# Optimization experiments

Measured on AMD Instinct MI355X. Metric: run time of the kernel, lower is better.

Reference implementation:

```python
import jax, jax.numpy as jnp
import numpy as np

N_NODES = 50000
N_EDGES = 1000000
D_IN = 128
HID = 64
N_GRAPHS = 256
NEG_SLOPE = 0.2


def _gatv2_layer(x, src, dst, Wl, Wr, att, b, n_nodes):
    # lin_l applied to source nodes, lin_r to target nodes (PyG GATv2Conv, heads=1)
    xl = x @ Wl.T  # [N, C]
    xr = x @ Wr.T  # [N, C]
    e = jax.nn.leaky_relu(xl[src] + xr[dst], NEG_SLOPE)  # [E, C]
    logits = e @ att  # [E]
    # segment softmax over destination node
    m = jax.ops.segment_max(logits, dst, num_segments=n_nodes)
    ex = jnp.exp(logits - m[dst])
    den = jax.ops.segment_sum(ex, dst, num_segments=n_nodes)
    alpha = ex / den[dst]  # [E]
    out = jax.ops.segment_sum(alpha[:, None] * xl[src], dst, num_segments=n_nodes)
    return out + b


def setup_inputs() -> dict:
    key = jax.random.key(0)
    ks = jax.random.split(key, 32)
    x = jax.random.normal(ks[0], (N_NODES, D_IN), dtype=jnp.float32)
    edge_index = jax.random.randint(ks[1], (2, N_EDGES), 0, N_NODES, dtype=jnp.int64)
    batch = jnp.sort(jax.random.randint(ks[2], (N_NODES,), 0, N_GRAPHS, dtype=jnp.int64))
    inp = {"x": x, "edge_index": edge_index, "batch": batch}
    dims = [D_IN, HID, HID]  # input dim per layer
    kidx = 3
    for i, din in enumerate(dims):
        inp[f"Wl{i}"] = jax.random.normal(ks[kidx], (HID, din), dtype=jnp.float32) * 0.1; kidx += 1
        inp[f"Wr{i}"] = jax.random.normal(ks[kidx], (HID, din), dtype=jnp.float32) * 0.1; kidx += 1
        inp[f"att{i}"] = jax.random.normal(ks[kidx], (HID,), dtype=jnp.float32) * 0.1; kidx += 1
        inp[f"b{i}"] = jnp.zeros((HID,), dtype=jnp.float32)
        inp[f"Rw{i}"] = jax.random.normal(ks[kidx], (HID, din), dtype=jnp.float32) * 0.1; kidx += 1
        inp[f"Rb{i}"] = jnp.zeros((HID,), dtype=jnp.float32)
    inp["Wf"] = jax.random.normal(ks[kidx], (1, HID), dtype=jnp.float32) * 0.1
    inp["bf"] = jnp.zeros((1,), dtype=jnp.float32)
    return inp


def reference(x, edge_index, batch, Wl0, Wr0, att0, b0, Rw0, Rb0,
              Wl1, Wr1, att1, b1, Rw1, Rb1,
              Wl2, Wr2, att2, b2, Rw2, Rb2, Wf, bf):
    n = x.shape[0]
    # add_self_loops=True (PyG default)
    loops = jnp.arange(n, dtype=edge_index.dtype)
    src = jnp.concatenate([edge_index[0], loops])
    dst = jnp.concatenate([edge_index[1], loops])
    layers = [(Wl0, Wr0, att0, b0, Rw0, Rb0),
              (Wl1, Wr1, att1, b1, Rw1, Rb1),
              (Wl2, Wr2, att2, b2, Rw2, Rb2)]
    for i, (Wl, Wr, att, b, Rw, Rb) in enumerate(layers):
        h = _gatv2_layer(x, src, dst, Wl, Wr, att, b, n) + (x @ Rw.T + Rb)  # res=True
        # norm=None -> Identity; dropout inactive at inference
        x = jax.nn.relu(h) if i < len(layers) - 1 else h
    # global_mean_pool
    sums = jax.ops.segment_sum(x, batch, num_segments=N_GRAPHS)
    cnt = jax.ops.segment_sum(jnp.ones((n,), x.dtype), batch, num_segments=N_GRAPHS)
    pooled = sums / jnp.maximum(cnt, 1.0)[:, None]
    return pooled @ Wf.T + bf
```

## Files before the change

### kernel.cpp

```cpp
#include <hip/hip_runtime.h>


#define NN 50000
#define NE 1000000
#define HID 64
#define DIN0 128
#define NG 256
#define NEG 0.2f

#define SCHUNK 1024
#define SNB ((NN + SCHUNK - 1) / SCHUNK)

typedef float f32x4 __attribute__((ext_vector_type(4)));
typedef short s8v __attribute__((ext_vector_type(8)));
typedef short s4v __attribute__((ext_vector_type(4)));
typedef __bf16 bf16x8 __attribute__((ext_vector_type(8)));
typedef _Float16 h2v __attribute__((ext_vector_type(2)));
typedef unsigned u32x2 __attribute__((ext_vector_type(2)));
typedef unsigned short u16;

__device__ __forceinline__ unsigned short f2bf(float f) {
    unsigned u = __float_as_uint(f);
    u = u + 0x7fffu + ((u >> 16) & 1u);
    return (unsigned short)(u >> 16);
}
__device__ __forceinline__ float bf2f(unsigned short v) {
    return __uint_as_float(((unsigned)v) << 16);
}
__device__ __forceinline__ short split_hi(float x) {
    return (short)f2bf(x);
}
__device__ __forceinline__ short split_lo(float x, short hi) {
    return (short)f2bf(x - bf2f((unsigned short)hi));
}
__device__ __forceinline__ h2v u2h(unsigned u) { return __builtin_bit_cast(h2v, u); }
__device__ __forceinline__ unsigned h2u(h2v h) { return __builtin_bit_cast(unsigned, h); }
__device__ __forceinline__ h2v pklo(unsigned a, unsigned b) {
    return u2h(__builtin_amdgcn_perm(b, a, 0x05040100u));
}
__device__ __forceinline__ h2v pkhi(unsigned a, unsigned b) {
    return u2h(__builtin_amdgcn_perm(b, a, 0x07060302u));
}
template <int CTRL>
__device__ __forceinline__ float dpp_mv(float v) {
    return __int_as_float(
        __builtin_amdgcn_update_dpp(0, __float_as_int(v), CTRL, 0xF, 0xF, true));
}
template <int OFF>
__device__ __forceinline__ float swz(float v) {
    return __int_as_float(__builtin_amdgcn_ds_swizzle(__float_as_int(v), OFF));
}
__device__ __forceinline__ float red32_add(float v) {
    unsigned u = __float_as_uint(v);
    u32x2 r = __builtin_amdgcn_permlane32_swap(u, u, false, false);
    return __uint_as_float(r[0]) + __uint_as_float(r[1]);
}
__device__ __forceinline__ float red32_max(float v) {
    unsigned u = __float_as_uint(v);
    u32x2 r = __builtin_amdgcn_permlane32_swap(u, u, false, false);
    return fmaxf(__uint_as_float(r[0]), __uint_as_float(r[1]));
}
__device__ __forceinline__ float octet_sum(float v) {
    v += dpp_mv<0xB1>(v);
    v += dpp_mv<0x4E>(v);
    v += swz<0x101F>(v);
    return v;
}
__device__ __forceinline__ float esum(float v) {
    v += dpp_mv<0x128>(v);
    v += swz<0x401F>(v);
    return red32_add(v);
}
__device__ __forceinline__ float emax(float v) {
    v = fmaxf(v, dpp_mv<0x128>(v));
    v = fmaxf(v, swz<0x401F>(v));
    return red32_max(v);
}

__global__ __launch_bounds__(256) void k_prep(
        const float* __restrict__ Wl0, const float* __restrict__ Wr0, const float* __restrict__ Rw0,
        const float* __restrict__ Wl1, const float* __restrict__ Wr1, const float* __restrict__ Rw1,
        const float* __restrict__ Wl2, const float* __restrict__ Wr2, const float* __restrict__ Rw2,
        const float* __restrict__ att0, const float* __restrict__ att1, const float* __restrict__ att2,
        short* __restrict__ Ws0, short* __restrict__ Ws1, short* __restrict__ Ws2,
        _Float16* __restrict__ attp,
        const int* __restrict__ batch,
        int* __restrict__ startg, int* __restrict__ endg,
        int* __restrict__ cnt8) {
    int i = blockIdx.x * 256 + threadIdx.x;
    if (i < 3 * HID) {
        int L = i >> 6, c = i & 63;
        const float* at = (L == 0) ? att0 : (L == 1) ? att1 : att2;
        float a = at[c];
        attp[L * 2 * HID + c] = (_Float16)(0.6f * a);
        attp[L * 2 * HID + HID + c] = (_Float16)(0.4f * a);
    }
    if (i < NN) {
#pragma unroll
        for (int g = 0; g < 8; g++) cnt8[g * NN + i] = 0;
        int g = batch[i];
        if (i == 0) {
            startg[g] = 0;
            for (int g2 = 0; g2 < g; g2++) { startg[g2] = 0; endg[g2] = 0; }
        } else if (batch[i - 1] != g) {
            startg[g] = i;
            for (int g2 = batch[i - 1] + 1; g2 < g; g2++) { startg[g2] = i; endg[g2] = i; }
        }
        if (i == NN - 1) {
            endg[g] = NN;
            for (int g2 = g + 1; g2 < NG; g2++) { startg[g2] = NN; endg[g2] = NN; }
        } else if (batch[i + 1] != g) {
            endg[g] = i + 1;
        }
    }
    const int L0N = 3 * HID * DIN0;
    const int L1N = 3 * HID * HID;
    if (i >= L0N + 2 * L1N) return;
    const float* Wm; short* Ws; int din, local;
    if (i < L0N) {
        local = i; din = DIN0; Ws = Ws0;
        int m = local / (DIN0 * HID);
        Wm = (m == 0) ? Wl0 : (m == 1) ? Wr0 : Rw0;
    } else if (i < L0N + L1N) {
        local = i - L0N; din = HID; Ws = Ws1;
        int m = local / (HID * HID);
        Wm = (m == 0) ? Wl1 : (m == 1) ? Wr1 : Rw1;
    } else {
        local = i - L0N - L1N; din = HID; Ws = Ws2;
        int m = local / (HID * HID);
        Wm = (m == 0) ? Wl2 : (m == 1) ? Wr2 : Rw2;
    }
    int m = local / (din * HID);
    int r = local - m * (din * HID);
    int c = r / din, k = r - c * din;
    float w = Wm[c * din + k];
    short hi = split_hi(w);
    short lo = split_lo(w, hi);
    Ws[(((m * 2 + 0) * HID + c) * din) + k] = hi;
    Ws[(((m * 2 + 1) * HID + c) * din) + k] = lo;
}

__global__ __launch_bounds__(256) void k_hist8(const int* __restrict__ edst,
                                               int* __restrict__ cnt8,
                                               u16* __restrict__ rank) {
    int* mycnt = cnt8 + (blockIdx.x & 7) * NN;
    for (int e = blockIdx.x * 256 + threadIdx.x; e < NE; e += 512 * 256) {
        int r = atomicAdd(&mycnt[edst[e]], 1);
        rank[e] = (u16)r;
    }
}

__global__ __launch_bounds__(256) void k_histscan(int* __restrict__ cnt8,
                                                  int* __restrict__ cnt,
                                                  int* __restrict__ part) {
    __shared__ int ws[4];
    int b = blockIdx.x, t = threadIdx.x;
    int i0 = b * SCHUNK + t * 4;
    int tot = 0;
#pragma unroll
    for (int j = 0; j < 4; j++) {
        int i = i0 + j;
        if (i < NN) {
            int s = 1;
#pragma unroll
            for (int g = 0; g < 8; g++) {
                int v = cnt8[g * NN + i];
                cnt8[g * NN + i] = s;
                s += v;
            }
            cnt[i] = s;
            tot += s;
        }
    }
#pragma unroll
    for (int o = 32; o; o >>= 1) tot += __shfl_xor(tot, o, 64);
    if ((t & 63) == 0) ws[t >> 6] = tot;
    __syncthreads();
    if (t == 0) part[b] = ws[0] + ws[1] + ws[2] + ws[3];
}

__global__ __launch_bounds__(256) void k_scan_emit(const int* __restrict__ cnt,
                                                   const int* __restrict__ part,
                                                   int* __restrict__ off,
                                                   u16* __restrict__ srcs) {
    __shared__ int tsum[256];
    __shared__ int baseSh;
    int b = blockIdx.x, t = threadIdx.x;
    if (t < 64) {
        int v = (t < b && t < SNB) ? part[t] : 0;
#pragma unroll
        for (int o = 32; o; o >>= 1) v += __shfl_xor(v, o, 64);
        if (t == 0) baseSh = v;
    }
    int i0 = b * SCHUNK + t * 4;
    int e[4], p[4];
    int s = 0;
#pragma unroll
    for (int j = 0; j < 4; j++) {
        int i = i0 + j;
        e[j] = (i < NN) ? cnt[i] : 0;
        p[j] = s;
        s += e[j];
    }
    tsum[t] = s;
    __syncthreads();
    for (int d = 1; d < 256; d <<= 1) {
        int v = (t >= d) ? tsum[t - d] : 0;
        __syncthreads();
        tsum[t] += v;
        __syncthreads();
    }
    int base = baseSh + ((t == 0) ? 0 : tsum[t - 1]);
#pragma unroll
    for (int j = 0; j < 4; j++) {
        int i = i0 + j;
        if (i < NN) {
            int v = base + p[j];
            off[i] = v;
            srcs[v] = (u16)i;
            if (i == NN - 1) off[NN] = v + e[j];
        }
    }
}

__global__ __launch_bounds__(256) void k_scatter_rank(
        const int* __restrict__ esrc, const int* __restrict__ edst,
        const int* __restrict__ off, const int* __restrict__ cnt8,
        const u16* __restrict__ rank, u16* __restrict__ srcs) {
    int e = blockIdx.x * 256 + threadIdx.x;
    if (e >= NE) return;
    int d = edst[e];
    int slice = (e >> 8) & 7;
    int pos = off[d] + cnt8[slice * NN + d] + (int)rank[e];
    srcs[pos] = (u16)esrc[e];
}

template <int DIN, bool RELU>
__global__ __launch_bounds__(256, 3) void k_gemm(
        const float* __restrict__ xin, const short* __restrict__ Ws,
        const float* __restrict__ bvec, const float* __restrict__ rb,
        _Float16* __restrict__ xl16, _Float16* __restrict__ xr16, float* __restrict__ acc) {
    constexpr int LROW = 40;
    __shared__ short lds[20480];
    short* xhi = lds;
    short* xlo = lds + 2560;

    const int tid = threadIdx.x;
    const int w = tid >> 6;
    const int lane = tid & 63;
    const int col = lane & 15;
    const int quad = lane >> 4;
    const int nb0 = blockIdx.x * 64;

    f32x4 d[3][4];
#pragma unroll
    for (int m = 0; m < 3; m++)
#pragma unroll
        for (int ct = 0; ct < 4; ct++) d[m][ct] = (f32x4){0.f, 0.f, 0.f, 0.f};

    for (int c0 = 0; c0 < DIN; c0 += 32) {
        if (c0) __syncthreads();
        for (int u = tid; u < 512; u += 256) {
            int row = u >> 3, kq = u & 7;
            int n = nb0 + row;
            float4 v = make_float4(0.f, 0.f, 0.f, 0.f);
            if (n < NN) {
                v = *(const float4*)&xin[(size_t)n * DIN + c0 + 4 * kq];
                if (RELU) {
                    v.x = fmaxf(v.x, 0.f); v.y = fmaxf(v.y, 0.f);
                    v.z = fmaxf(v.z, 0.f); v.w = fmaxf(v.w, 0.f);
                }
            }
            s4v h, l;
            short h0 = split_hi(v.x), l0 = split_lo(v.x, h0);
            short h1 = split_hi(v.y), l1 = split_lo(v.y, h1);
            short h2 = split_hi(v.z), l2 = split_lo(v.z, h2);
            short h3 = split_hi(v.w), l3 = split_lo(v.w, h3);
            h[0] = h0; h[1] = h1; h[2] = h2; h[3] = h3;
            l[0] = l0; l[1] = l1; l[2] = l2; l[3] = l3;
            *(s4v*)&xhi[row * LROW + 4 * kq] = h;
            *(s4v*)&xlo[row * LROW + 4 * kq] = l;
        }
        for (int u = tid; u < 1536; u += 256) {
            int mp = u >> 8;
            int r = u & 255;
            int c = r >> 2, q = r & 3;
            s8v v = *(const s8v*)&Ws[((mp * HID + c) * DIN) + c0 + 8 * q];
            *(s8v*)&lds[5120 + mp * 2560 + c * LROW + 8 * q] = v;
        }
        __syncthreads();

        bf16x8 a_h = __builtin_bit_cast(bf16x8,
            *(const s8v*)&xhi[(w * 16 + col) * LROW + quad * 8]);
        bf16x8 a_l = __builtin_bit_cast(bf16x8,
            *(const s8v*)&xlo[(w * 16 + col) * LROW + quad * 8]);

#pragma unroll
        for (int m = 0; m < 3; m++) {
#pragma unroll
            for (int ct = 0; ct < 4; ct++) {
                bf16x8 b_h = __builtin_bit_cast(bf16x8,
                    *(const s8v*)&lds[5120 + (m * 2 + 0) * 2560 + (ct * 16 + col) * LROW + quad * 8]);
                bf16x8 b_l = __builtin_bit_cast(bf16x8,
                    *(const s8v*)&lds[5120 + (m * 2 + 1) * 2560 + (ct * 16 + col) * LROW + quad * 8]);
                d[m][ct] = __builtin_amdgcn_mfma_f32_16x16x32_bf16(a_h, b_h, d[m][ct], 0, 0, 0);
                d[m][ct] = __builtin_amdgcn_mfma_f32_16x16x32_bf16(a_h, b_l, d[m][ct], 0, 0, 0);
                d[m][ct] = __builtin_amdgcn_mfma_f32_16x16x32_bf16(a_l, b_h, d[m][ct], 0, 0, 0);
            }
        }
    }

#pragma unroll
    for (int r = 0; r < 4; r++) {
        int n = nb0 + w * 16 + quad * 4 + r;
        if (n >= NN) continue;
        size_t base = (size_t)n * HID;
#pragma unroll
        for (int ct = 0; ct < 4; ct++) {
            int c = ct * 16 + col;
            xl16[base + c] = (_Float16)d[0][ct][r];
            xr16[base + c] = (_Float16)d[1][ct][r];
            acc[base + c] = d[2][ct][r] + bvec[c] + rb[c];
        }
    }
}

__global__ __launch_bounds__(256) void k_attn_dst(
        const int* __restrict__ off, const u16* __restrict__ srcs,
        const _Float16* __restrict__ xl16, const _Float16* __restrict__ xr16,
        const _Float16* __restrict__ attL, float* __restrict__ acc) {
    const int lane = threadIdx.x & 63;
    const int d0 = blockIdx.x * 8 + (threadIdx.x >> 6) * 2;
    const int d1 = d0 + 1;
    const int e = lane >> 3;
    const int cg = lane & 7;

    const int lo0 = off[d0], deg0 = off[d0 + 1] - lo0;
    const int lo1 = off[d1], deg1 = off[d1 + 1] - lo1;

    uint4 X0 = *(const uint4*)&xr16[(size_t)d0 * HID + 8 * cg];
    uint4 X1 = *(const uint4*)&xr16[(size_t)d1 * HID + 8 * cg];
    uint4 A6 = *(const uint4*)&attL[8 * cg];
    uint4 A4 = *(const uint4*)&attL[HID + 8 * cg];
    h2v x00 = u2h(X0.x), x01 = u2h(X0.y), x02 = u2h(X0.z), x03 = u2h(X0.w);
    h2v x10 = u2h(X1.x), x11 = u2h(X1.y), x12 = u2h(X1.z), x13 = u2h(X1.w);
    h2v a60 = u2h(A6.x), a61 = u2h(A6.y), a62 = u2h(A6.z), a63 = u2h(A6.w);
    h2v a40 = u2h(A4.x), a41 = u2h(A4.y), a42 = u2h(A4.z), a43 = u2h(A4.w);

#define GATHER(S) (*(const uint4*)&xl16[(size_t)(S) * HID + 8 * cg])
#define LOGIT(U, XH0, XH1, XH2, XH3, T)                                        \
    {                                                                          \
        h2v _v; unsigned _a; float _q0, _q1;                                   \
        _v = u2h(U.x) + XH0; _a = h2u(_v) & 0x7FFF7FFFu;                       \
        _q0 = __builtin_amdgcn_fdot2(a60, _v, 0.f, false);                     \
        _q1 = __builtin_amdgcn_fdot2(a40, u2h(_a), 0.f, false);                \
        _v = u2h(U.y) + XH1; _a = h2u(_v) & 0x7FFF7FFFu;                       \
        _q0 = __builtin_amdgcn_fdot2(a61, _v, _q0, false);                     \
        _q1 = __builtin_amdgcn_fdot2(a41, u2h(_a), _q1, false);                \
        _v = u2h(U.z) + XH2; _a = h2u(_v) & 0x7FFF7FFFu;                       \
        _q0 = __builtin_amdgcn_fdot2(a62, _v, _q0, false);                     \
        _q1 = __builtin_amdgcn_fdot2(a42, u2h(_a), _q1, false);                \
        _v = u2h(U.w) + XH3; _a = h2u(_v) & 0x7FFF7FFFu;                       \
        _q0 = __builtin_amdgcn_fdot2(a63, _v, _q0, false);                     \
        _q1 = __builtin_amdgcn_fdot2(a43, u2h(_a), _q1, false);                \
        T = octet_sum(_q0 + _q1);                                              \
    }
#define PVACC(P, Ua, Ub, OA, OB)                                               \
    OA.x = __builtin_amdgcn_fdot2(P, pklo(Ua.x, Ub.x), OA.x, false);           \
    OA.y = __builtin_amdgcn_fdot2(P, pkhi(Ua.x, Ub.x), OA.y, false);           \
    OA.z = __builtin_amdgcn_fdot2(P, pklo(Ua.y, Ub.y), OA.z, false);           \
    OA.w = __builtin_amdgcn_fdot2(P, pkhi(Ua.y, Ub.y), OA.w, false);           \
    OB.x = __builtin_amdgcn_fdot2(P, pklo(Ua.z, Ub.z), OB.x, false);           \
    OB.y = __builtin_amdgcn_fdot2(P, pkhi(Ua.z, Ub.z), OB.y, false);           \
    OB.z = __builtin_amdgcn_fdot2(P, pklo(Ua.w, Ub.w), OB.z, false);           \
    OB.w = __builtin_amdgcn_fdot2(P, pkhi(Ua.w, Ub.w), OB.w, false);

    int s00 = (int)srcs[lo0 + min(e, deg0 - 1)];
    int s01 = (int)srcs[lo0 + min(8 + e, deg0 - 1)];
    int s02 = (int)srcs[lo0 + min(16 + e, deg0 - 1)];
    int s03 = (int)srcs[lo0 + min(24 + e, deg0 - 1)];
    int s10 = (int)srcs[lo1 + min(e, deg1 - 1)];
    int s11 = (int)srcs[lo1 + min(8 + e, deg1 - 1)];
    int s12 = (int)srcs[lo1 + min(16 + e, deg1 - 1)];
    int s13 = (int)srcs[lo1 + min(24 + e, deg1 - 1)];
    const bool a2 = deg0 > 16, a3 = deg0 > 24;
    const bool b2 = deg1 > 16, b3 = deg1 > 24;

    uint4 U00 = GATHER(s00), U01 = GATHER(s01);
    uint4 U10 = GATHER(s10), U11 = GATHER(s11);
    uint4 U02, U03, U12, U13;
    float t00, t01, t02 = -INFINITY, t03 = -INFINITY;
    float t10, t11, t12 = -INFINITY, t13 = -INFINITY;
    if (a2) {
        U02 = GATHER(s02);
        if (a3) U03 = GATHER(s03); else U03 = U00;
    }
    if (b2) {
        U12 = GATHER(s12);
        if (b3) U13 = GATHER(s13); else U13 = U10;
    }
    LOGIT(U00, x00, x01, x02, x03, t00);
    LOGIT(U01, x00, x01, x02, x03, t01);
    LOGIT(U10, x10, x11, x12, x13, t10);
    LOGIT(U11, x10, x11, x12, x13, t11);
    if (e >= deg0) t00 = -INFINITY;
    if (8 + e >= deg0) t01 = -INFINITY;
    if (e >= deg1) t10 = -INFINITY;
    if (8 + e >= deg1) t11 = -INFINITY;
    if (a2) {
        LOGIT(U02, x00, x01, x02, x03, t02);
        if (16 + e >= deg0) t02 = -INFINITY;
        if (a3) {
            LOGIT(U03, x00, x01, x02, x03, t03);
            if (24 + e >= deg0) t03 = -INFINITY;
        }
    }
    if (b2) {
        LOGIT(U12, x10, x11, x12, x13, t12);
        if (16 + e >= deg1) t12 = -INFINITY;
        if (b3) {
            LOGIT(U13, x10, x11, x12, x13, t13);
            if (24 + e >= deg1) t13 = -INFINITY;
        }
    }

    float m0 = emax(fmaxf(fmaxf(t00, t01), fmaxf(t02, t03)));
    float m1 = emax(fmaxf(fmaxf(t10, t11), fmaxf(t12, t13)));

    float p00 = __expf(t00 - m0), p01 = __expf(t01 - m0);
    float p10 = __expf(t10 - m1), p11 = __expf(t11 - m1);
    float l0 = p00 + p01, l1 = p10 + p11;
    float4 oA0 = make_float4(0.f, 0.f, 0.f, 0.f), oB0 = oA0;
    float4 oA1 = oA0, oB1 = oA0;
    {
        h2v pa = {(_Float16)p00, (_Float16)p01};
        h2v pb = {(_Float16)p10, (_Float16)p11};
        PVACC(pa, U00, U01, oA0, oB0)
        PVACC(pb, U10, U11, oA1, oB1)
    }
    if (a2) {
        float p02 = __expf(t02 - m0), p03 = __expf(t03 - m0);
        l0 += p02 + p03;
        h2v pa = {(_Float16)p02, (_Float16)p03};
        PVACC(pa, U02, U03, oA0, oB0)
    }
    if (b2) {
        float p12 = __expf(t12 - m1), p13 = __expf(t13 - m1);
        l1 += p12 + p13;
        h2v pb = {(_Float16)p12, (_Float16)p13};
        PVACC(pb, U12, U13, oA1, oB1)
    }

#define GENLOOP(LO, DEG, XH0, XH1, XH2, XH3, M, L, OA, OB)                     \
    for (int base = 32; base < DEG; base += 32) {                              \
        const int rem = DEG - base;                                            \
        int s0 = (int)srcs[LO + min(base + e, DEG - 1)];                       \
        int s1 = (int)srcs[LO + min(base + 8 + e, DEG - 1)];                   \
        int s2 = (int)srcs[LO + min(base + 16 + e, DEG - 1)];                  \
        int s3 = (int)srcs[LO + min(base + 24 + e, DEG - 1)];                  \
        uint4 V0 = GATHER(s0), V1 = GATHER(s1), V2, V3;                        \
        float u0, u1, u2 = -INFINITY, u3 = -INFINITY;                          \
        LOGIT(V0, XH0, XH1, XH2, XH3, u0);                                     \
        LOGIT(V1, XH0, XH1, XH2, XH3, u1);                                     \
        if (base + e >= DEG) u0 = -INFINITY;                                   \
        if (base + 8 + e >= DEG) u1 = -INFINITY;                               \
        const bool c2 = rem > 16;                                              \
        if (c2) {                                                              \
            V2 = GATHER(s2);                                                   \
            LOGIT(V2, XH0, XH1, XH2, XH3, u2);                                 \
            if (base + 16 + e >= DEG) u2 = -INFINITY;                          \
            if (rem > 24) {                                                    \
                V3 = GATHER(s3);                                               \
                LOGIT(V3, XH0, XH1, XH2, XH3, u3);                             \
                if (base + 24 + e >= DEG) u3 = -INFINITY;                      \
            } else { V3 = V0; }                                                \
        }                                                                      \
        float cm = emax(fmaxf(fmaxf(u0, u1), fmaxf(u2, u3)));                  \
        if (cm > M) {                                                          \
            float corr = __expf(M - cm);                                       \
            M = cm;                                                            \
            L *= corr;                                                         \
            OA.x *= corr; OA.y *= corr; OA.z *= corr; OA.w *= corr;            \
            OB.x *= corr; OB.y *= corr; OB.z *= corr; OB.w *= corr;            \
        }                                                                      \
        float q0 = __expf(u0 - M), q1 = __expf(u1 - M);                        \
        L += q0 + q1;                                                          \
        h2v qp = {(_Float16)q0, (_Float16)q1};                                 \
        PVACC(qp, V0, V1, OA, OB)                                              \
        if (c2) {                                                              \
            float q2 = __expf(u2 - M), q3 = __expf(u3 - M);                    \
            L += q2 + q3;                                                      \
            h2v qq = {(_Float16)q2, (_Float16)q3};                             \
            PVACC(qq, V2, V3, OA, OB)                                          \
        }                                                                      \
    }

    if (deg0 > 32) { GENLOOP(lo0, deg0, x00, x01, x02, x03, m0, l0, oA0, oB0) }
    if (deg1 > 32) { GENLOOP(lo1, deg1, x10, x11, x12, x13, m1, l1, oA1, oB1) }
#undef GENLOOP
#undef GATHER
#undef LOGIT
#undef PVACC

    l0    = esum(l0);    l1    = esum(l1);
    oA0.x = esum(oA0.x); oA1.x = esum(oA1.x);
    oA0.y = esum(oA0.y); oA1.y = esum(oA1.y);
    oA0.z = esum(oA0.z); oA1.z = esum(oA1.z);
    oA0.w = esum(oA0.w); oA1.w = esum(oA1.w);
    oB0.x = esum(oB0.x); oB1.x = esum(oB1.x);
    oB0.y = esum(oB0.y); oB1.y = esum(oB1.y);
    oB0.z = esum(oB0.z); oB1.z = esum(oB1.z);
    oB0.w = esum(oB0.w); oB1.w = esum(oB1.w);

    if (e < 2) {
        const bool s = (e == 1);
        int dd = s ? d1 : d0;
        float inv = 1.f / (s ? l1 : l0);
        float4 wA = s ? oA1 : oA0;
        float4 wB = s ? oB1 : oB0;
        float4* a4 = (float4*)&acc[(size_t)dd * HID + 8 * cg];
        float4 c0 = a4[0], c1 = a4[1];
        c0.x += wA.x * inv; c0.y += wA.y * inv;
        c0.z += wA.z * inv; c0.w += wA.w * inv;
        c1.x += wB.x * inv; c1.y += wB.y * inv;
        c1.z += wB.z * inv; c1.w += wB.w * inv;
        a4[0] = c0; a4[1] = c1;
    }
}

__global__ __launch_bounds__(512) void k_pool_final(
        const float* __restrict__ acc,
        const int* __restrict__ startg, const int* __restrict__ endg,
        const float* __restrict__ Wf, const float* __restrict__ bf_,
        float* __restrict__ out) {
    __shared__ float red[8][HID];
    const int g = blockIdx.x;
    const int c = threadIdx.x & 63;
    const int j = threadIdx.x >> 6;
    const int s = startg[g], epos = endg[g];

    float sum = 0.f;
    for (int n = s + j; n < epos; n += 8)
        sum += acc[(size_t)n * HID + c];
    red[j][c] = sum;
    __syncthreads();

    if (threadIdx.x < HID) {
        float tot = 0.f;
#pragma unroll
        for (int w = 0; w < 8; w++) tot += red[w][c];
        float cntf = (float)(epos - s);
        float v = tot / fmaxf(cntf, 1.f) * Wf[c];
#pragma unroll
        for (int o = 32; o; o >>= 1) v += __shfl_xor(v, o, 64);
        if (c == 0) out[g] = v + bf_[0];
    }
}

extern "C" void kernel_launch(void* const* d_in, const int* in_sizes, int n_in,
                              void* d_out, int out_size, void* d_ws, size_t ws_size,
                              hipStream_t stream) {
    const float* x   = (const float*)d_in[0];
    const int* eidx  = (const int*)d_in[1];
    const int* batch = (const int*)d_in[2];
    const int* esrc = eidx;
    const int* edst = eidx + NE;
    const float* Wf  = (const float*)d_in[21];
    const float* bfb = (const float*)d_in[22];

    float* wsf = (float*)d_ws;
    const size_t NN64 = (size_t)NN * HID;
    _Float16* xl16 = (_Float16*)wsf;
    _Float16* xr16 = (_Float16*)(wsf + NN64);
    float* acc0   = wsf + 2 * NN64;
    float* acc1   = acc0 + NN64;
    short* Ws0    = (short*)(acc1 + NN64);
    short* Ws1    = Ws0 + 2 * 3 * HID * DIN0;
    short* Ws2    = Ws1 + 2 * 3 * HID * HID;
    int*   ccnt   = (int*)(Ws2 + 2 * 3 * HID * HID);
    int*   startg = ccnt + NN;
    int*   endg   = startg + NG;
    int*   off    = endg + NG;
    int*   part   = off + NN + 1;
    int*   partSc = part + SNB;
    int*   cnt8   = partSc + SNB;
    u16*   rank   = (u16*)(cnt8 + 8 * NN);
    u16*   srcs   = rank + NE;
    _Float16* attp = (_Float16*)(srcs + NE + NN);

    k_prep<<<(NN + 255) / 256, 256, 0, stream>>>(
        (const float*)d_in[3], (const float*)d_in[4], (const float*)d_in[7],
        (const float*)d_in[9], (const float*)d_in[10], (const float*)d_in[13],
        (const float*)d_in[15], (const float*)d_in[16], (const float*)d_in[19],
        (const float*)d_in[5], (const float*)d_in[11], (const float*)d_in[17],
        Ws0, Ws1, Ws2, attp, batch, startg, endg, cnt8);

    k_hist8<<<512, 256, 0, stream>>>(edst, cnt8, rank);
    k_histscan<<<SNB, 256, 0, stream>>>(cnt8, ccnt, part);
    k_scan_emit<<<SNB, 256, 0, stream>>>(ccnt, part, off, srcs);
    k_scatter_rank<<<(NE + 255) / 256, 256, 0, stream>>>(esrc, edst, off, cnt8, rank, srcs);

    const short* Wss[3] = {Ws0, Ws1, Ws2};
    float* accs[4] = {acc0, acc0, acc1, acc0};
    const int gemm_grid = (NN + 63) / 64;
    for (int L = 0; L < 3; L++) {
        const float* b   = (const float*)d_in[3 + L * 6 + 3];
        const float* Rb  = (const float*)d_in[3 + L * 6 + 5];
        float* accOut = accs[L + 1];

        if (L == 0)
            k_gemm<DIN0, false><<<gemm_grid, 256, 0, stream>>>(
                x, Wss[0], b, Rb, xl16, xr16, accOut);
        else
            k_gemm<HID, true><<<gemm_grid, 256, 0, stream>>>(
                accs[L], Wss[L], b, Rb, xl16, xr16, accOut);

        k_attn_dst<<<NN / 8, 256, 0, stream>>>(
            off, srcs, xl16, xr16, attp + L * 2 * HID, accOut);
    }

    k_pool_final<<<NG, 512, 0, stream>>>(accs[3], startg, endg, Wf, bfb, (float*)d_out);
}
```

Baseline: 312.1 us.

## Fuse layer-0 GEMM with destination histogram into one heterogeneous launch

```diff
diff --git a/kernel.cpp b/kernel.cpp
--- a/kernel.cpp
+++ b/kernel.cpp
@@ -10,6 +10,8 @@
 
 #define SCHUNK 1024
 #define SNB ((NN + SCHUNK - 1) / SCHUNK)
+#define G0B ((NN + 63) / 64)
+#define HB 512
 
 typedef float f32x4 __attribute__((ext_vector_type(4)));
 typedef short s8v __attribute__((ext_vector_type(8)));
@@ -140,104 +142,9 @@
     Ws[(((m * 2 + 1) * HID + c) * din) + k] = lo;
 }
 
-__global__ __launch_bounds__(256) void k_hist8(const int* __restrict__ edst,
-                                               int* __restrict__ cnt8,
-                                               u16* __restrict__ rank) {
-    int* mycnt = cnt8 + (blockIdx.x & 7) * NN;
-    for (int e = blockIdx.x * 256 + threadIdx.x; e < NE; e += 512 * 256) {
-        int r = atomicAdd(&mycnt[edst[e]], 1);
-        rank[e] = (u16)r;
-    }
-}
-
-__global__ __launch_bounds__(256) void k_histscan(int* __restrict__ cnt8,
-                                                  int* __restrict__ cnt,
-                                                  int* __restrict__ part) {
-    __shared__ int ws[4];
-    int b = blockIdx.x, t = threadIdx.x;
-    int i0 = b * SCHUNK + t * 4;
-    int tot = 0;
-#pragma unroll
-    for (int j = 0; j < 4; j++) {
-        int i = i0 + j;
-        if (i < NN) {
-            int s = 1;
-#pragma unroll
-            for (int g = 0; g < 8; g++) {
-                int v = cnt8[g * NN + i];
-                cnt8[g * NN + i] = s;
-                s += v;
-            }
-            cnt[i] = s;
-            tot += s;
-        }
-    }
-#pragma unroll
-    for (int o = 32; o; o >>= 1) tot += __shfl_xor(tot, o, 64);
-    if ((t & 63) == 0) ws[t >> 6] = tot;
-    __syncthreads();
-    if (t == 0) part[b] = ws[0] + ws[1] + ws[2] + ws[3];
-}
-
-__global__ __launch_bounds__(256) void k_scan_emit(const int* __restrict__ cnt,
-                                                   const int* __restrict__ part,
-                                                   int* __restrict__ off,
-                                                   u16* __restrict__ srcs) {
-    __shared__ int tsum[256];
-    __shared__ int baseSh;
-    int b = blockIdx.x, t = threadIdx.x;
-    if (t < 64) {
-        int v = (t < b && t < SNB) ? part[t] : 0;
-#pragma unroll
-        for (int o = 32; o; o >>= 1) v += __shfl_xor(v, o, 64);
-        if (t == 0) baseSh = v;
-    }
-    int i0 = b * SCHUNK + t * 4;
-    int e[4], p[4];
-    int s = 0;
-#pragma unroll
-    for (int j = 0; j < 4; j++) {
-        int i = i0 + j;
-        e[j] = (i < NN) ? cnt[i] : 0;
-        p[j] = s;
-        s += e[j];
-    }
-    tsum[t] = s;
-    __syncthreads();
-    for (int d = 1; d < 256; d <<= 1) {
-        int v = (t >= d) ? tsum[t - d] : 0;
-        __syncthreads();
-        tsum[t] += v;
-        __syncthreads();
-    }
-    int base = baseSh + ((t == 0) ? 0 : tsum[t - 1]);
-#pragma unroll
-    for (int j = 0; j < 4; j++) {
-        int i = i0 + j;
-        if (i < NN) {
-            int v = base + p[j];
-            off[i] = v;
-            srcs[v] = (u16)i;
-            if (i == NN - 1) off[NN] = v + e[j];
-        }
-    }
-}
-
-__global__ __launch_bounds__(256) void k_scatter_rank(
-        const int* __restrict__ esrc, const int* __restrict__ edst,
-        const int* __restrict__ off, const int* __restrict__ cnt8,
-        const u16* __restrict__ rank, u16* __restrict__ srcs) {
-    int e = blockIdx.x * 256 + threadIdx.x;
-    if (e >= NE) return;
-    int d = edst[e];
-    int slice = (e >> 8) & 7;
-    int pos = off[d] + cnt8[slice * NN + d] + (int)rank[e];
-    srcs[pos] = (u16)esrc[e];
-}
-
 template <int DIN, bool RELU>
-__global__ __launch_bounds__(256, 3) void k_gemm(
-        const float* __restrict__ xin, const short* __restrict__ Ws,
+__device__ __forceinline__ void gemm_body(
+        int nb0, const float* __restrict__ xin, const short* __restrict__ Ws,
         const float* __restrict__ bvec, const float* __restrict__ rb,
         _Float16* __restrict__ xl16, _Float16* __restrict__ xr16, float* __restrict__ acc) {
     constexpr int LROW = 40;
@@ -250,7 +157,6 @@
     const int lane = tid & 63;
     const int col = lane & 15;
     const int quad = lane >> 4;
-    const int nb0 = blockIdx.x * 64;
 
     f32x4 d[3][4];
 #pragma unroll
@@ -323,6 +229,116 @@
             acc[base + c] = d[2][ct][r] + bvec[c] + rb[c];
         }
     }
+}
+
+__global__ __launch_bounds__(256, 3) void k_g0_hist(
+        const float* __restrict__ xin, const short* __restrict__ Ws,
+        const float* __restrict__ bvec, const float* __restrict__ rb,
+        _Float16* __restrict__ xl16, _Float16* __restrict__ xr16, float* __restrict__ acc,
+        const int* __restrict__ edst, int* __restrict__ cnt8, u16* __restrict__ rank) {
+    if (blockIdx.x < G0B) {
+        gemm_body<DIN0, false>(blockIdx.x * 64, xin, Ws, bvec, rb, xl16, xr16, acc);
+    } else {
+        int b = blockIdx.x - G0B;
+        int* mycnt = cnt8 + (b & 7) * NN;
+        for (int e = b * 256 + threadIdx.x; e < NE; e += HB * 256) {
+            int r = atomicAdd(&mycnt[edst[e]], 1);
+            rank[e] = (u16)r;
+        }
+    }
+}
+
+template <int DIN, bool RELU>
+__global__ __launch_bounds__(256, 3) void k_gemm(
+        const float* __restrict__ xin, const short* __restrict__ Ws,
+        const float* __restrict__ bvec, const float* __restrict__ rb,
+        _Float16* __restrict__ xl16, _Float16* __restrict__ xr16, float* __restrict__ acc) {
+    gemm_body<DIN, RELU>(blockIdx.x * 64, xin, Ws, bvec, rb, xl16, xr16, acc);
+}
+
+__global__ __launch_bounds__(256) void k_histscan(int* __restrict__ cnt8,
+                                                  int* __restrict__ cnt,
+                                                  int* __restrict__ part) {
+    __shared__ int ws[4];
+    int b = blockIdx.x, t = threadIdx.x;
+    int i0 = b * SCHUNK + t * 4;
+    int tot = 0;
+#pragma unroll
+    for (int j = 0; j < 4; j++) {
+        int i = i0 + j;
+        if (i < NN) {
+            int s = 1;
+#pragma unroll
+            for (int g = 0; g < 8; g++) {
+                int v = cnt8[g * NN + i];
+                cnt8[g * NN + i] = s;
+                s += v;
+            }
+            cnt[i] = s;
+            tot += s;
+        }
+    }
+#pragma unroll
+    for (int o = 32; o; o >>= 1) tot += __shfl_xor(tot, o, 64);
+    if ((t & 63) == 0) ws[t >> 6] = tot;
+    __syncthreads();
+    if (t == 0) part[b] = ws[0] + ws[1] + ws[2] + ws[3];
+}
+
+__global__ __launch_bounds__(256) void k_scan_emit(const int* __restrict__ cnt,
+                                                   const int* __restrict__ part,
+                                                   int* __restrict__ off,
+                                                   u16* __restrict__ srcs) {
+    __shared__ int tsum[256];
+    __shared__ int baseSh;
+    int b = blockIdx.x, t = threadIdx.x;
+    if (t < 64) {
+        int v = (t < b && t < SNB) ? part[t] : 0;
+#pragma unroll
+        for (int o = 32; o; o >>= 1) v += __shfl_xor(v, o, 64);
+        if (t == 0) baseSh = v;
+    }
+    int i0 = b * SCHUNK + t * 4;
+    int e[4], p[4];
+    int s = 0;
+#pragma unroll
+    for (int j = 0; j < 4; j++) {
+        int i = i0 + j;
+        e[j] = (i < NN) ? cnt[i] : 0;
+        p[j] = s;
+        s += e[j];
+    }
+    tsum[t] = s;
+    __syncthreads();
+    for (int d = 1; d < 256; d <<= 1) {
+        int v = (t >= d) ? tsum[t - d] : 0;
+        __syncthreads();
+        tsum[t] += v;
+        __syncthreads();
+    }
+    int base = baseSh + ((t == 0) ? 0 : tsum[t - 1]);
+#pragma unroll
+    for (int j = 0; j < 4; j++) {
+        int i = i0 + j;
+        if (i < NN) {
+            int v = base + p[j];
+            off[i] = v;
+            srcs[v] = (u16)i;
+            if (i == NN - 1) off[NN] = v + e[j];
+        }
+    }
+}
+
+__global__ __launch_bounds__(256) void k_scatter_rank(
+        const int* __restrict__ esrc, const int* __restrict__ edst,
+        const int* __restrict__ off, const int* __restrict__ cnt8,
+        const u16* __restrict__ rank, u16* __restrict__ srcs) {
+    int e = blockIdx.x * 256 + threadIdx.x;
+    if (e >= NE) return;
+    int d = edst[e];
+    int slice = (e >> 8) & 7;
+    int pos = off[d] + cnt8[slice * NN + d] + (int)rank[e];
+    srcs[pos] = (u16)esrc[e];
 }
 
 __global__ __launch_bounds__(256) void k_attn_dst(
@@ -595,7 +611,10 @@
         (const float*)d_in[5], (const float*)d_in[11], (const float*)d_in[17],
         Ws0, Ws1, Ws2, attp, batch, startg, endg, cnt8);
 
-    k_hist8<<<512, 256, 0, stream>>>(edst, cnt8, rank);
+    k_g0_hist<<<G0B + HB, 256, 0, stream>>>(
+        x, Ws0, (const float*)d_in[6], (const float*)d_in[8],
+        xl16, xr16, acc0, edst, cnt8, rank);
+
     k_histscan<<<SNB, 256, 0, stream>>>(cnt8, ccnt, part);
     k_scan_emit<<<SNB, 256, 0, stream>>>(ccnt, part, off, srcs);
     k_scatter_rank<<<(NE + 255) / 256, 256, 0, stream>>>(esrc, edst, off, cnt8, rank, srcs);
@@ -608,10 +627,7 @@
         const float* Rb  = (const float*)d_in[3 + L * 6 + 5];
         float* accOut = accs[L + 1];
 
-        if (L == 0)
-            k_gemm<DIN0, false><<<gemm_grid, 256, 0, stream>>>(
-                x, Wss[0], b, Rb, xl16, xr16, accOut);
-        else
+        if (L > 0)
             k_gemm<HID, true><<<gemm_grid, 256, 0, stream>>>(
                 accs[L], Wss[L], b, Rb, xl16, xr16, accOut);
 
```

Measured after the change: 295.8 us, median of 3. -5.2%, faster.
